# Performance work log

Measured on AMD Instinct MI355X. Metric: run time of the kernel, lower is better.

Reference implementation:

```python
import jax, jax.numpy as jnp
import numpy as np

N_NODES = 100000
N_EDGES = 1600000
IN_CH = 64
HID = 64
OUT_CH = 128
EDGE_CH = 3
OBS_RANGE = 0.5
ATK_RANGE = 0.3


def setup_inputs() -> dict:
    key = jax.random.key(0)
    k = jax.random.split(key, 8)
    # node features: first column is an integer node type in {0,1,2}
    node_type = jax.random.randint(k[0], (N_NODES, 1), 0, 3).astype(jnp.float32)
    feats = jax.random.normal(k[1], (N_NODES, IN_CH - 1), dtype=jnp.float32)
    x = jnp.concatenate([node_type, feats], axis=-1)
    edge_index = jax.random.randint(k[2], (2, N_EDGES), 0, N_NODES)
    # edge_attr[:,0] = distance in [0,1)
    edge_attr = jax.random.uniform(k[3], (N_EDGES, EDGE_CH), dtype=jnp.float32)
    s1 = 1.0 / np.sqrt(2 * IN_CH + EDGE_CH)
    s2 = 1.0 / np.sqrt(HID)
    W1 = jax.random.normal(k[4], (2 * IN_CH + EDGE_CH, HID), dtype=jnp.float32) * s1
    b1 = jnp.zeros((HID,), dtype=jnp.float32)
    W2 = jax.random.normal(k[5], (HID, OUT_CH), dtype=jnp.float32) * s2
    b2 = jnp.zeros((OUT_CH,), dtype=jnp.float32)
    return {"x": x, "edge_index": edge_index, "edge_attr": edge_attr,
            "W1": W1, "b1": b1, "W2": W2, "b2": b2}


def reference(x, edge_index, edge_attr, W1, b1, W2, b2):
    src = edge_index[0]  # j (source)
    dst = edge_index[1]  # i (target)
    x_j = x[src]         # [E, IN_CH]
    x_i = x[dst]         # [E, IN_CH]
    h = jnp.concatenate([x_i, x_j, edge_attr], axis=-1)  # [E, 2*IN_CH+3]
    msg = jax.nn.relu(h @ W1 + b1) @ W2 + b2             # [E, OUT_CH]
    dist = edge_attr[:, 0]
    ntype = x_j[:, 0]
    mask = jnp.where(ntype == 0, dist < OBS_RANGE,
                     jnp.where(ntype == 1, dist < ATK_RANGE, True))
    msg = mask[:, None].astype(msg.dtype) * msg
    out = jax.ops.segment_sum(msg, dst, num_segments=x.shape[0])  # [N, OUT_CH]
    return jax.nn.relu(out)
```

## Files before the change

### kernel.cpp

```cpp
#include <hip/hip_runtime.h>

#define N_NODES 100000
#define N_EDGES 1600000
#define IN_CH   64
#define HID_CH  64
#define OUT_CH  128
#define TILE    128
#define N_TILES (N_EDGES / TILE)

typedef __attribute__((ext_vector_type(8))) __bf16    bf16x8;
typedef __attribute__((ext_vector_type(4))) float     f32x4;
typedef __attribute__((ext_vector_type(2))) _Float16  f16x2;
typedef __attribute__((ext_vector_type(8))) _Float16  f16x8;

__device__ __forceinline__ unsigned short f2bf(float f) {
    union { float f; unsigned int i; } c;
    c.f = f;
    unsigned int u = c.i;
    unsigned int r = (u + 0x7FFFu + ((u >> 16) & 1u)) >> 16;
    return (unsigned short)r;
}

__device__ __forceinline__ void atomic_pk_add_f16(unsigned int* addr, f16x2 val) {
    typedef __attribute__((address_space(1))) f16x2 gf16x2;
    __builtin_amdgcn_global_atomic_fadd_v2f16((gf16x2*)(void*)addr, val);
}

__global__ void gnn_prep(const float* __restrict__ xf,
                         unsigned short* __restrict__ xb,
                         unsigned char* __restrict__ ntype,
                         uint4* __restrict__ hz,
                         float4* __restrict__ cz) {
    int i = blockIdx.x * blockDim.x + threadIdx.x;
    if (i < 1600000) {
        float4 v = reinterpret_cast<const float4*>(xf)[i];
        ushort4 o;
        o.x = f2bf(v.x); o.y = f2bf(v.y); o.z = f2bf(v.z); o.w = f2bf(v.w);
        reinterpret_cast<ushort4*>(xb)[i] = o;
        if ((i & 15) == 0) {
            int n = i >> 4;
            ntype[n] = (v.x == 0.0f) ? 0 : ((v.x == 1.0f) ? 1 : 2);
        }
    } else if (i < 2400000) {
        hz[i - 1600000] = (uint4){0u, 0u, 0u, 0u};
    } else if (i < 2425000) {
        cz[i - 2400000] = (float4){0.f, 0.f, 0.f, 0.f};
    }
}

__global__ __launch_bounds__(256, 4) void gnn_edge_hidden(
    const unsigned char*  __restrict__ ntype,
    const unsigned short* __restrict__ xb,
    const int*            __restrict__ eidx,
    const float*          __restrict__ ea,
    const float*          __restrict__ W1,
    const float*          __restrict__ b1,
    unsigned int*         __restrict__ hsum,
    float*                __restrict__ cnt)
{
    __shared__ __align__(16) unsigned short W1T[64][136];
    __shared__ float w1tail[4][64];
    __shared__ float eas[128][4];
    __shared__ float masks[128];
    __shared__ int   dsts[128];
    __shared__ int   srcs[128];

    const int tid  = threadIdx.x;
    const int wave = tid >> 6;
    const int lane = tid & 63;
    const int q    = lane >> 4;
    const int m16  = lane & 15;

    for (int idx = tid; idx < 128 * 64; idx += 256) {
        int k = idx >> 6, n = idx & 63;
        W1T[n][k] = f2bf(W1[idx]);
    }
    if (tid < 64) {
        w1tail[0][tid] = W1[128 * 64 + tid];
        w1tail[1][tid] = W1[129 * 64 + tid];
        w1tail[2][tid] = W1[130 * 64 + tid];
        w1tail[3][tid] = b1[tid];
    }

    for (int t = blockIdx.x; t < N_TILES; t += gridDim.x) {
        __syncthreads();
        if (tid < 128) {
            int e = t * TILE + tid;
            int s = eidx[e];
            int d = eidx[N_EDGES + e];
            srcs[tid] = s;
            dsts[tid] = d;
            float a0 = ea[e * 3 + 0];
            float a1 = ea[e * 3 + 1];
            float a2 = ea[e * 3 + 2];
            eas[tid][0] = a0; eas[tid][1] = a1; eas[tid][2] = a2;
            int ntc = ntype[s];
            float mk;
            if (ntc == 0)      mk = (a0 < 0.5f) ? 1.0f : 0.0f;
            else if (ntc == 1) mk = (a0 < 0.3f) ? 1.0f : 0.0f;
            else               mk = 1.0f;
            masks[tid] = mk;
            if (mk != 0.0f) unsafeAtomicAdd(&cnt[d], 1.0f);
        }
        __syncthreads();

        const int ebase = wave * 32;

        f32x4 acc1[2][4];
#pragma unroll
        for (int mt = 0; mt < 2; ++mt) {
            float e0[4], e1[4], e2[4];
#pragma unroll
            for (int r = 0; r < 4; ++r) {
                int el = ebase + mt * 16 + q * 4 + r;
                e0[r] = eas[el][0]; e1[r] = eas[el][1]; e2[r] = eas[el][2];
            }
#pragma unroll
            for (int nt = 0; nt < 4; ++nt) {
                int n = nt * 16 + m16;
                float t0 = w1tail[0][n], t1 = w1tail[1][n];
                float t2 = w1tail[2][n], bb = w1tail[3][n];
#pragma unroll
                for (int r = 0; r < 4; ++r)
                    acc1[mt][nt][r] = bb + e0[r] * t0 + e1[r] * t1 + e2[r] * t2;
            }
        }

#pragma unroll
        for (int kc = 0; kc < 4; ++kc) {
            bf16x8 af[2];
#pragma unroll
            for (int mt = 0; mt < 2; ++mt) {
                int el   = ebase + mt * 16 + m16;
                int node = (kc < 2) ? dsts[el] : srcs[el];
                af[mt] = *reinterpret_cast<const bf16x8*>(
                    xb + (size_t)node * IN_CH + (kc & 1) * 32 + q * 8);
            }
#pragma unroll
            for (int nt = 0; nt < 4; ++nt) {
                bf16x8 bfr = *reinterpret_cast<const bf16x8*>(
                    &W1T[nt * 16 + m16][kc * 32 + q * 8]);
                acc1[0][nt] = __builtin_amdgcn_mfma_f32_16x16x32_bf16(af[0], bfr, acc1[0][nt], 0, 0, 0);
                acc1[1][nt] = __builtin_amdgcn_mfma_f32_16x16x32_bf16(af[1], bfr, acc1[1][nt], 0, 0, 0);
            }
        }

#pragma unroll
        for (int mt = 0; mt < 2; ++mt) {
#pragma unroll
            for (int r = 0; r < 4; ++r) {
                int el = ebase + mt * 16 + q * 4 + r;
                float mk = masks[el];
                if (mk != 0.0f) {
                    unsigned int* hbase = hsum + (size_t)dsts[el] * 32;
                    float v0 = acc1[mt][0][r]; v0 = v0 > 0.f ? v0 : 0.f;
                    float v1 = acc1[mt][1][r]; v1 = v1 > 0.f ? v1 : 0.f;
                    float v2 = acc1[mt][2][r]; v2 = v2 > 0.f ? v2 : 0.f;
                    float v3 = acc1[mt][3][r]; v3 = v3 > 0.f ? v3 : 0.f;
                    if (v0 + v1 > 0.f) {
                        f16x2 p01 = {(_Float16)v0, (_Float16)v1};
                        atomic_pk_add_f16(hbase + m16, p01);
                    }
                    if (v2 + v3 > 0.f) {
                        f16x2 p23 = {(_Float16)v2, (_Float16)v3};
                        atomic_pk_add_f16(hbase + 16 + m16, p23);
                    }
                }
            }
        }
    }
}

__global__ __launch_bounds__(256, 4) void gnn_node_out(
    const _Float16* __restrict__ hsum,
    const float*    __restrict__ cnt,
    const float*    __restrict__ W2,
    const float*    __restrict__ b2,
    float*          __restrict__ out)
{
    __shared__ __align__(16) unsigned short W2T[128][72];
    __shared__ float b2s[128];

    const int tid  = threadIdx.x;
    const int wave = tid >> 6;
    const int lane = tid & 63;
    const int q    = lane >> 4;
    const int m16  = lane & 15;

    for (int idx = tid; idx < 64 * 128; idx += 256) {
        int p = idx >> 7, n = idx & 127;
        int ch = (p >> 1) + 16 * (p & 1) + ((p >= 32) ? 16 : 0);
        W2T[n][p] = f2bf(W2[ch * 128 + n]);
    }
    if (tid < 128) b2s[tid] = b2[tid];
    __syncthreads();

    const int nodeBase = (blockIdx.x * 4 + wave) * 32;
    if (nodeBase >= N_NODES) return;

    f32x4 acc[2][8];
#pragma unroll
    for (int mt = 0; mt < 2; ++mt)
#pragma unroll
        for (int nt = 0; nt < 8; ++nt)
            acc[mt][nt] = (f32x4){0.0f, 0.0f, 0.0f, 0.0f};

#pragma unroll
    for (int kc = 0; kc < 2; ++kc) {
        bf16x8 af[2];
#pragma unroll
        for (int mt = 0; mt < 2; ++mt) {
            int node = nodeBase + mt * 16 + m16;
            if (node >= N_NODES) node = N_NODES - 1;
            f16x8 h = *reinterpret_cast<const f16x8*>(
                hsum + (size_t)node * HID_CH + kc * 32 + q * 8);
            union { bf16x8 v; unsigned short u[8]; } rr;
#pragma unroll
            for (int j = 0; j < 8; ++j) rr.u[j] = f2bf((float)h[j]);
            af[mt] = rr.v;
        }
#pragma unroll
        for (int nt = 0; nt < 8; ++nt) {
            bf16x8 bfr = *reinterpret_cast<const bf16x8*>(
                &W2T[nt * 16 + m16][kc * 32 + q * 8]);
            acc[0][nt] = __builtin_amdgcn_mfma_f32_16x16x32_bf16(af[0], bfr, acc[0][nt], 0, 0, 0);
            acc[1][nt] = __builtin_amdgcn_mfma_f32_16x16x32_bf16(af[1], bfr, acc[1][nt], 0, 0, 0);
        }
    }

#pragma unroll
    for (int mt = 0; mt < 2; ++mt) {
        float cc[4]; int nn[4];
#pragma unroll
        for (int r = 0; r < 4; ++r) {
            nn[r] = nodeBase + mt * 16 + q * 4 + r;
            cc[r] = (nn[r] < N_NODES) ? cnt[nn[r]] : 0.0f;
        }
#pragma unroll
        for (int nt = 0; nt < 8; ++nt) {
            int col = nt * 16 + m16;
            float bb = b2s[col];
#pragma unroll
            for (int r = 0; r < 4; ++r) {
                if (nn[r] < N_NODES) {
                    float v = acc[mt][nt][r] + cc[r] * bb;
                    out[(size_t)nn[r] * OUT_CH + col] = v > 0.0f ? v : 0.0f;
                }
            }
        }
    }
}

extern "C" void kernel_launch(void* const* d_in, const int* in_sizes, int n_in,
                              void* d_out, int out_size, void* d_ws, size_t ws_size,
                              hipStream_t stream) {
    const float* x  = (const float*)d_in[0];
    const int*   ei = (const int*)d_in[1];
    const float* ea = (const float*)d_in[2];
    const float* W1 = (const float*)d_in[3];
    const float* b1 = (const float*)d_in[4];
    const float* W2 = (const float*)d_in[5];
    const float* b2 = (const float*)d_in[6];
    float* out = (float*)d_out;

    char* wsb = (char*)d_ws;
    unsigned int*   hsum  = (unsigned int*)wsb;
    float*          cnt   = (float*)(wsb + 12800000);
    unsigned short* xb    = (unsigned short*)(wsb + 13200000);
    unsigned char*  ntype = (unsigned char*)(wsb + 26000000);

    gnn_prep<<<(2425000 + 255) / 256, 256, 0, stream>>>(
        x, xb, ntype, (uint4*)hsum, (float4*)cnt);

    gnn_edge_hidden<<<1792, 256, 0, stream>>>(ntype, xb, ei, ea, W1, b1, hsum, cnt);

    gnn_node_out<<<(N_NODES + 127) / 128, 256, 0, stream>>>(
        (const _Float16*)hsum, cnt, W2, b2, out);
}
```

Measured before the change: 279.8 us.

## Make edge-tile staging wave-local and drop block barriers in edge kernel

Each wave now loads its own 32 edges' indices, attributes and mask into shared memory, so the two per-tile __syncthreads are gone. The mask is packed into the sign bit of the destination index. Masked edges point their source gather at node 0, which keeps those loads cheap. The W1 tail weights and bias move into the padding of the transposed W1 tile and are read as one float4. The change also raises launch bounds to 8 blocks per CU, grows the grid to 2048 blocks, and raises wave priority around the MFMA block; the higher occupancy target risks register pressure or spills.

```diff
diff --git a/kernel.cpp b/kernel.cpp
--- a/kernel.cpp
+++ b/kernel.cpp
@@ -48,7 +48,7 @@
     }
 }
 
-__global__ __launch_bounds__(256, 4) void gnn_edge_hidden(
+__global__ __launch_bounds__(256, 8) void gnn_edge_hidden(
     const unsigned char*  __restrict__ ntype,
     const unsigned short* __restrict__ xb,
     const int*            __restrict__ eidx,
@@ -59,10 +59,8 @@
     float*                __restrict__ cnt)
 {
     __shared__ __align__(16) unsigned short W1T[64][136];
-    __shared__ float w1tail[4][64];
-    __shared__ float eas[128][4];
-    __shared__ float masks[128];
-    __shared__ int   dsts[128];
+    __shared__ float eas[128][3];
+    __shared__ int   dstm[128];
     __shared__ int   srcs[128];
 
     const int tid  = threadIdx.x;
@@ -76,35 +74,33 @@
         W1T[n][k] = f2bf(W1[idx]);
     }
     if (tid < 64) {
-        w1tail[0][tid] = W1[128 * 64 + tid];
-        w1tail[1][tid] = W1[129 * 64 + tid];
-        w1tail[2][tid] = W1[130 * 64 + tid];
-        w1tail[3][tid] = b1[tid];
-    }
+        float4 tl;
+        tl.x = W1[128 * 64 + tid];
+        tl.y = W1[129 * 64 + tid];
+        tl.z = W1[130 * 64 + tid];
+        tl.w = b1[tid];
+        *reinterpret_cast<float4*>(&W1T[tid][128]) = tl;
+    }
+    __syncthreads();
+
+    const int ebase = wave * 32;
 
     for (int t = blockIdx.x; t < N_TILES; t += gridDim.x) {
-        __syncthreads();
-        if (tid < 128) {
-            int e = t * TILE + tid;
+        if (lane < 32) {
+            int e  = t * TILE + ebase + lane;
+            int el = ebase + lane;
             int s = eidx[e];
             int d = eidx[N_EDGES + e];
-            srcs[tid] = s;
-            dsts[tid] = d;
             float a0 = ea[e * 3 + 0];
             float a1 = ea[e * 3 + 1];
             float a2 = ea[e * 3 + 2];
-            eas[tid][0] = a0; eas[tid][1] = a1; eas[tid][2] = a2;
+            eas[el][0] = a0; eas[el][1] = a1; eas[el][2] = a2;
             int ntc = ntype[s];
-            float mk;
-            if (ntc == 0)      mk = (a0 < 0.5f) ? 1.0f : 0.0f;
-            else if (ntc == 1) mk = (a0 < 0.3f) ? 1.0f : 0.0f;
-            else               mk = 1.0f;
-            masks[tid] = mk;
-            if (mk != 0.0f) unsafeAtomicAdd(&cnt[d], 1.0f);
-        }
-        __syncthreads();
-
-        const int ebase = wave * 32;
+            bool mk = (ntc == 0) ? (a0 < 0.5f) : ((ntc == 1) ? (a0 < 0.3f) : true);
+            dstm[el] = mk ? (int)(0x80000000u | (unsigned)d) : 0;
+            srcs[el] = mk ? s : 0;
+            if (mk) unsafeAtomicAdd(&cnt[d], 1.0f);
+        }
 
         f32x4 acc1[2][4];
 #pragma unroll
@@ -118,11 +114,10 @@
 #pragma unroll
             for (int nt = 0; nt < 4; ++nt) {
                 int n = nt * 16 + m16;
-                float t0 = w1tail[0][n], t1 = w1tail[1][n];
-                float t2 = w1tail[2][n], bb = w1tail[3][n];
+                float4 wt = *reinterpret_cast<const float4*>(&W1T[n][128]);
 #pragma unroll
                 for (int r = 0; r < 4; ++r)
-                    acc1[mt][nt][r] = bb + e0[r] * t0 + e1[r] * t1 + e2[r] * t2;
+                    acc1[mt][nt][r] = wt.w + e0[r] * wt.x + e1[r] * wt.y + e2[r] * wt.z;
             }
         }
 
@@ -131,11 +126,13 @@
             bf16x8 af[2];
 #pragma unroll
             for (int mt = 0; mt < 2; ++mt) {
-                int el   = ebase + mt * 16 + m16;
-                int node = (kc < 2) ? dsts[el] : srcs[el];
+                int el = ebase + mt * 16 + m16;
+                int dm = dstm[el];
+                int node = (kc < 2) ? (dm & 0x7FFFFFFF) : srcs[el];
                 af[mt] = *reinterpret_cast<const bf16x8*>(
                     xb + (size_t)node * IN_CH + (kc & 1) * 32 + q * 8);
             }
+            __builtin_amdgcn_s_setprio(1);
 #pragma unroll
             for (int nt = 0; nt < 4; ++nt) {
                 bf16x8 bfr = *reinterpret_cast<const bf16x8*>(
@@ -143,6 +140,7 @@
                 acc1[0][nt] = __builtin_amdgcn_mfma_f32_16x16x32_bf16(af[0], bfr, acc1[0][nt], 0, 0, 0);
                 acc1[1][nt] = __builtin_amdgcn_mfma_f32_16x16x32_bf16(af[1], bfr, acc1[1][nt], 0, 0, 0);
             }
+            __builtin_amdgcn_s_setprio(0);
         }
 
 #pragma unroll
@@ -150,9 +148,9 @@
 #pragma unroll
             for (int r = 0; r < 4; ++r) {
                 int el = ebase + mt * 16 + q * 4 + r;
-                float mk = masks[el];
-                if (mk != 0.0f) {
-                    unsigned int* hbase = hsum + (size_t)dsts[el] * 32;
+                int dm = dstm[el];
+                if (dm < 0) {
+                    unsigned int* hbase = hsum + (size_t)(dm & 0x7FFFFFFF) * 32;
                     float v0 = acc1[mt][0][r]; v0 = v0 > 0.f ? v0 : 0.f;
                     float v1 = acc1[mt][1][r]; v1 = v1 > 0.f ? v1 : 0.f;
                     float v2 = acc1[mt][2][r]; v2 = v2 > 0.f ? v2 : 0.f;
@@ -272,7 +270,7 @@
     gnn_prep<<<(2425000 + 255) / 256, 256, 0, stream>>>(
         x, xb, ntype, (uint4*)hsum, (float4*)cnt);
 
-    gnn_edge_hidden<<<1792, 256, 0, stream>>>(ntype, xb, ei, ea, W1, b1, hsum, cnt);
+    gnn_edge_hidden<<<2048, 256, 0, stream>>>(ntype, xb, ei, ea, W1, b1, hsum, cnt);
 
     gnn_node_out<<<(N_NODES + 127) / 128, 256, 0, stream>>>(
         (const _Float16*)hsum, cnt, W2, b2, out);
```

Measured after the change: 576.9 us. 106% more time.
